# Optimization experiments

Measured on AMD Instinct MI355X. Metric: run time of the kernel, lower is better.

## Reference

```python
import jax, jax.numpy as jnp
import numpy as np

DIM = 128
HEADS = 8
HEAD_DIM = DIM // HEADS
K = 5          # kernel_size per spatial axis
DIL = 1        # dilation
EPS = 1e-5


def setup_inputs() -> dict:
    key = jax.random.key(0)
    ks = jax.random.split(key, 12)
    s = 0.02
    inp = {
        "x": jax.random.normal(ks[0], (1, DIM, 16, 16, 4), jnp.float32),
        "skip": jax.random.normal(ks[1], (1, DIM, 32, 32, 8), jnp.float32),
        "Wq": jax.random.normal(ks[2], (DIM, DIM), jnp.float32) * s,
        "bq": jnp.zeros((DIM,), jnp.float32),
        "Wk": jax.random.normal(ks[3], (DIM, DIM), jnp.float32) * s,
        "bk": jnp.zeros((DIM,), jnp.float32),
        "Wv": jax.random.normal(ks[4], (DIM, DIM), jnp.float32) * s,
        "bv": jnp.zeros((DIM,), jnp.float32),
        "rpb": jax.random.normal(ks[5], (HEADS, 2 * K - 1, 2 * K - 1, 2 * K - 1), jnp.float32) * s,
        "Wo": jax.random.normal(ks[6], (DIM, DIM), jnp.float32) * s,
        "bo": jnp.zeros((DIM,), jnp.float32),
    }
    return inp


def _instance_norm(t):
    # InstanceNorm3d, affine=False: normalize over spatial dims per (B, C)
    mu = jnp.mean(t, axis=(2, 3, 4), keepdims=True)
    var = jnp.var(t, axis=(2, 3, 4), keepdims=True)
    return (t - mu) * jax.lax.rsqrt(var + EPS)


def _nbr_idx(L):
    # NATTEN-style clamped window: start shifted to stay in bounds
    i = np.arange(L)
    start = np.clip(i - (K // 2) * DIL, 0, L - 1 - (K - 1) * DIL)
    idx = start[:, None] + np.arange(K)[None, :] * DIL  # (L, K)
    rel = (idx - i[:, None]) // DIL + (K - 1)           # (L, K) in [0, 2K-2]
    return jnp.asarray(idx), jnp.asarray(rel)


def reference(x, skip, Wq, bq, Wk, bk, Wv, bv, rpb, Wo, bo):
    x = _instance_norm(x)
    skip = _instance_norm(skip)

    xu = jnp.repeat(jnp.repeat(jnp.repeat(x, 2, axis=2), 2, axis=3), 2, axis=4)

    B, C, H, W, Z = skip.shape
    N = H * W * Z
    xt = xu.transpose(0, 2, 3, 4, 1).reshape(B, N, C)    # queries from upsampled x
    st = skip.transpose(0, 2, 3, 4, 1).reshape(B, N, C)  # keys/values from skip

    def heads(t):
        return t.reshape(B, N, HEADS, HEAD_DIM).transpose(0, 2, 1, 3)  # (B,h,N,d)

    q = heads(xt @ Wq + bq) * (HEAD_DIM ** -0.5)
    k = heads(st @ Wk + bk)
    v = heads(st @ Wv + bv)

    idxH, relH = _nbr_idx(H)
    idxW, relW = _nbr_idx(W)
    idxZ, relZ = _nbr_idx(Z)

    # flattened neighbor token indices: (N, K^3)
    nbr = (idxH[:, None, None, :, None, None] * (W * Z)
           + idxW[None, :, None, None, :, None] * Z
           + idxZ[None, None, :, None, None, :])
    nbr = jnp.broadcast_to(nbr, (H, W, Z, K, K, K)).reshape(N, K ** 3)

    # relative position bias gather: (heads, N, K^3)
    rH = jnp.broadcast_to(relH[:, None, None, :, None, None], (H, W, Z, K, K, K)).reshape(N, K ** 3)
    rW = jnp.broadcast_to(relW[None, :, None, None, :, None], (H, W, Z, K, K, K)).reshape(N, K ** 3)
    rZ = jnp.broadcast_to(relZ[None, None, :, None, None, :], (H, W, Z, K, K, K)).reshape(N, K ** 3)
    bias = rpb[:, rH, rW, rZ]  # (heads, N, K^3)

    kg = jnp.take(k, nbr, axis=2)  # (B, h, N, K^3, d)
    vg = jnp.take(v, nbr, axis=2)

    logits = jnp.einsum('bhnd,bhnkd->bhnk', q, kg) + bias[None]
    attn = jax.nn.softmax(logits, axis=-1)
    out = jnp.einsum('bhnk,bhnkd->bhnd', attn, vg)

    out = out.transpose(0, 2, 1, 3).reshape(B, N, C) @ Wo + bo
    return out.reshape(B, H, W, Z, C).transpose(0, 4, 1, 2, 3)
```

## Files before the change

### kernel.cpp

```cpp
#include <hip/hip_runtime.h>
#include <math.h>

#define DIM 128
#define HEADS 8
#define HD 16
#define NPOS 8192
#define EPS 1e-5f

typedef _Float16 half2_t __attribute__((ext_vector_type(2)));
typedef _Float16 f16x8  __attribute__((ext_vector_type(8)));
typedef float    f32x4  __attribute__((ext_vector_type(4)));

static __device__ __forceinline__ half2_t u2h(unsigned u) {
    half2_t r; __builtin_memcpy(&r, &u, 4); return r;
}
static __device__ __forceinline__ unsigned pkh(float a, float b) {
    half2_t h; h.x = (_Float16)a; h.y = (_Float16)b;
    unsigned u; __builtin_memcpy(&u, &h, 4); return u;
}
static __device__ __forceinline__ float dot2(unsigned k, unsigned q, float acc) {
#if __has_builtin(__builtin_amdgcn_fdot2)
    return __builtin_amdgcn_fdot2(u2h(k), u2h(q), acc, false);
#else
    half2_t kh = u2h(k), qh = u2h(q);
    acc = fmaf((float)kh.x, (float)qh.x, acc);
    return fmaf((float)kh.y, (float)qh.y, acc);
#endif
}

__global__ __launch_bounds__(256) void stats_kernel(const float* __restrict__ x,
                                                    const float* __restrict__ skip,
                                                    const float* __restrict__ Wq,
                                                    const float* __restrict__ Wk,
                                                    const float* __restrict__ Wv,
                                                    const float* __restrict__ Wo,
                                                    float* __restrict__ ws,
                                                    unsigned short* __restrict__ Wt) {
    int c = blockIdx.x;
    int t = threadIdx.x;
    if (c >= 256) {
        int c2 = c - 256;
        int m = c2 >> 2, chunk = c2 & 3;
        const float* Wsrc = (m == 0) ? Wq : (m == 1) ? Wk : (m == 2) ? Wv : Wo;
        unsigned short* dst = Wt + (size_t)m * 16384;
        int co = t & 127, half = t >> 7;
        int ci0 = chunk * 32 + half * 16;
        unsigned pk8[8];
        #pragma unroll
        for (int j = 0; j < 8; ++j) {
            float a = Wsrc[(ci0 + 2*j    ) * 128 + co];
            float b = Wsrc[(ci0 + 2*j + 1) * 128 + co];
            pk8[j] = pkh(a, b);
        }
        *(uint4*)(dst + (size_t)co * 128 + ci0)     = *(uint4*)&pk8[0];
        *(uint4*)(dst + (size_t)co * 128 + ci0 + 8) = *(uint4*)&pk8[4];
        return;
    }
    const float* src; int n; float* mu_out; float* rs_out; int ci;
    if (c < DIM) { ci = c; src = x + c * 1024; n = 1024; mu_out = ws; rs_out = ws + DIM; }
    else { ci = c - DIM; src = skip + (size_t)ci * NPOS; n = NPOS; mu_out = ws + 2*DIM; rs_out = ws + 3*DIM; }
    const float4* s4 = (const float4*)src;
    int n4 = n >> 2;
    float s = 0.f, s2 = 0.f;
    for (int i = t; i < n4; i += 256) {
        float4 v = s4[i];
        s += (v.x + v.y) + (v.z + v.w);
        s2 = fmaf(v.x, v.x, fmaf(v.y, v.y, fmaf(v.z, v.z, fmaf(v.w, v.w, s2))));
    }
    #pragma unroll
    for (int off = 32; off > 0; off >>= 1) {
        s  += __shfl_down(s,  off, 64);
        s2 += __shfl_down(s2, off, 64);
    }
    __shared__ float ls[4], ls2[4];
    int wv = t >> 6;
    if ((t & 63) == 0) { ls[wv] = s; ls2[wv] = s2; }
    __syncthreads();
    if (t == 0) {
        float S  = ls[0] + ls[1] + ls[2] + ls[3];
        float S2 = ls2[0] + ls2[1] + ls2[2] + ls2[3];
        float inv_n = 1.f / (float)n;
        float mu  = S * inv_n;
        float var = S2 * inv_n - mu * mu;
        mu_out[ci] = mu;
        rs_out[ci] = rsqrtf(var + EPS);
    }
}

__global__ __launch_bounds__(256) void gemm_kernel(int phase,
    const float* __restrict__ x, const float* __restrict__ skip,
    const float* __restrict__ ao_t,
    const unsigned short* __restrict__ Wt_all,
    const float* __restrict__ bq, const float* __restrict__ bk,
    const float* __restrict__ bv, const float* __restrict__ bo,
    const float* __restrict__ ws,
    unsigned* __restrict__ q_out, unsigned* __restrict__ k_out,
    unsigned* __restrict__ v_out, float* __restrict__ out) {
    __shared__ __align__(16) unsigned short A_lds[32 * 128];
    int bx = blockIdx.x;
    const float* A; int lda; const float* mu; const float* rs;
    const unsigned short* Wt; const float* bias; float scale = 1.f;
    unsigned* opk = nullptr; float* of = nullptr; int n0;
    if (phase == 0) {
        if (bx < 256)      { A = skip; lda = NPOS; mu = ws + 256; rs = ws + 384;
                             Wt = Wt_all + 16384;     bias = bk; opk = k_out; n0 = bx * 32; }
        else if (bx < 512) { A = skip; lda = NPOS; mu = ws + 256; rs = ws + 384;
                             Wt = Wt_all + 2 * 16384; bias = bv; opk = v_out; n0 = (bx - 256) * 32; }
        else               { A = x;    lda = 1024; mu = ws;       rs = ws + 128;
                             Wt = Wt_all;             bias = bq; opk = q_out; n0 = (bx - 512) * 32;
                             scale = 0.25f; }
    } else {
        A = ao_t; lda = NPOS; mu = nullptr; rs = nullptr;
        Wt = Wt_all + 3 * 16384; bias = bo; of = out; n0 = bx * 32;
    }
    int t = threadIdx.x;
    int lane = t & 63, w = t >> 6;

    int co_f = w * 32 + (lane & 15);
    int kf   = (lane >> 4) * 8;
    uint4 wf[2][4];
    #pragma unroll
    for (int mt = 0; mt < 2; ++mt)
        #pragma unroll
        for (int k4 = 0; k4 < 4; ++k4)
            wf[mt][k4] = *(const uint4*)(Wt + (size_t)(co_f + mt * 16) * 128 + k4 * 32 + kf);

    {
        int pos = t & 31, g = t >> 5;
        const float* ap = A + n0 + pos;
        float f[16];
        #pragma unroll
        for (int rep = 0; rep < 4; ++rep) {
            int ci0 = g * 4 + rep * 32;
            f[rep*4+0] = ap[(size_t)(ci0    ) * lda];
            f[rep*4+1] = ap[(size_t)(ci0 + 1) * lda];
            f[rep*4+2] = ap[(size_t)(ci0 + 2) * lda];
            f[rep*4+3] = ap[(size_t)(ci0 + 3) * lda];
        }
        #pragma unroll
        for (int rep = 0; rep < 4; ++rep) {
            int ci0 = g * 4 + rep * 32;
            float f0 = f[rep*4+0], f1 = f[rep*4+1], f2 = f[rep*4+2], f3 = f[rep*4+3];
            if (phase == 0) {
                f0 = (f0 - mu[ci0    ]) * rs[ci0    ];
                f1 = (f1 - mu[ci0 + 1]) * rs[ci0 + 1];
                f2 = (f2 - mu[ci0 + 2]) * rs[ci0 + 2];
                f3 = (f3 - mu[ci0 + 3]) * rs[ci0 + 3];
            }
            int byte = (pos * 256 + ci0 * 2) ^ ((pos & 7) << 4);
            *(uint2*)((char*)A_lds + byte) = make_uint2(pkh(f0, f1), pkh(f2, f3));
        }
    }
    __syncthreads();

    f32x4 acc[2][2];
    #pragma unroll
    for (int mt = 0; mt < 2; ++mt)
        #pragma unroll
        for (int nt = 0; nt < 2; ++nt)
            acc[mt][nt] = (f32x4){0.f, 0.f, 0.f, 0.f};
    #pragma unroll
    for (int k4 = 0; k4 < 4; ++k4) {
        f16x8 af[2];
        #pragma unroll
        for (int nt = 0; nt < 2; ++nt) {
            int pos = nt * 16 + (lane & 15);
            int byte = (pos * 256 + (k4 * 32 + kf) * 2) ^ ((pos & 7) << 4);
            uint4 u = *(const uint4*)((const char*)A_lds + byte);
            __builtin_memcpy(&af[nt], &u, 16);
        }
        #pragma unroll
        for (int mt = 0; mt < 2; ++mt) {
            f16x8 wfr; __builtin_memcpy(&wfr, &wf[mt][k4], 16);
            acc[mt][0] = __builtin_amdgcn_mfma_f32_16x16x32_f16(wfr, af[0], acc[mt][0], 0, 0, 0);
            acc[mt][1] = __builtin_amdgcn_mfma_f32_16x16x32_f16(wfr, af[1], acc[mt][1], 0, 0, 0);
        }
    }

    int colp  = lane & 15;
    int rquad = (lane >> 4) * 4;
    #pragma unroll
    for (int mt = 0; mt < 2; ++mt) {
        int co = w * 32 + mt * 16 + rquad;
        float4 bv4 = *(const float4*)(bias + co);
        #pragma unroll
        for (int nt = 0; nt < 2; ++nt) {
            int pos = n0 + nt * 16 + colp;
            float v0 = (acc[mt][nt][0] + bv4.x) * scale;
            float v1 = (acc[mt][nt][1] + bv4.y) * scale;
            float v2 = (acc[mt][nt][2] + bv4.z) * scale;
            float v3 = (acc[mt][nt][3] + bv4.w) * scale;
            if (phase == 0) {
                *(uint2*)(opk + (size_t)pos * 64 + (co >> 1)) = make_uint2(pkh(v0, v1), pkh(v2, v3));
            } else {
                of[(size_t)(co    ) * NPOS + pos] = v0;
                of[(size_t)(co + 1) * NPOS + pos] = v1;
                of[(size_t)(co + 2) * NPOS + pos] = v2;
                of[(size_t)(co + 3) * NPOS + pos] = v3;
            }
        }
    }
}

__global__ __launch_bounds__(512, 4) void attn_kernel(const unsigned* __restrict__ qb,
                                                      const unsigned* __restrict__ kb,
                                                      const unsigned* __restrict__ vb,
                                                      const float* __restrict__ rpb,
                                                      float* __restrict__ ao_t) {
    __shared__ uint4 kbf[2 * 544];
    __shared__ uint4 vbf[2 * 544];
    __shared__ float bias_l[744];

    int blk = blockIdx.x;
    int h    = blk & 7;
    int tile = blk >> 3;
    int h0 = (tile >> 3) * 4;
    int w0 = (tile & 7) * 4;
    int bh0 = min(max(h0 - 2, 0), 24);
    int bw0 = min(max(w0 - 2, 0), 24);
    int t = threadIdx.x;

    for (int idx = t; idx < 1024; idx += 512) {
        int c2 = idx & 1;
        int r  = idx >> 1;
        int gz = r & 7;
        int q2 = r >> 3;
        int gh = q2 >> 3, gw = q2 & 7;
        int n = (bh0 + gh) * 256 + (bw0 + gw) * 8 + gz;
        int base = gh * 68 + gw * 8 + ((gz + gw) & 7);
        kbf[c2 * 544 + base] = *(const uint4*)(kb + (size_t)n * 64 + h * 8 + c2 * 4);
        vbf[c2 * 544 + base] = *(const uint4*)(vb + (size_t)n * 64 + h * 8 + c2 * 4);
    }
    for (int idx = t; idx < 744; idx += 512) bias_l[idx] = (idx < 729) ? rpb[h * 729 + idx] : 0.f;
    __syncthreads();

    int s = t & 7, p = t >> 3;
    int ph = p >> 4, pw = (p >> 2) & 3, pzp = p & 3;
    int hc = h0 + ph, wc = w0 + pw, zc0 = pzp * 2;
    int sh = min(max(hc - 2, 0), 27);
    int sw = min(max(wc - 2, 0), 27);
    int sz0 = min(max(zc0 - 2, 0), 3);
    int sz1 = min(max(zc0 - 1, 0), 3);
    int dlt = sz1 - sz0;
    int hb = sh - bh0, wb = sw - bw0;
    int b0 = (sh - hc + 4) * 81 + (sw - wc + 4) * 9 + (sz0 - zc0 + 4);
    int n0pos = hc * 256 + wc * 8 + zc0;

    int qrow = (hc >> 1) * 64 + (wc >> 1) * 4 + pzp;
    uint4 qa = *(const uint4*)(qb + (size_t)qrow * 64 + h * 8);
    uint4 qc = *(const uint4*)(qb + (size_t)qrow * 64 + h * 8 + 4);

    float o0[16], o1[16];
    #pragma unroll
    for (int d = 0; d < 16; ++d) { o0[d] = 0.f; o1[d] = 0.f; }
    float l0 = 0.f, l1 = 0.f;

    int cnt   = 18 + (s < 6);
    int start = s * 18 + min(s, 6);
    int i0 = p & 15;

    for (int it = 0; it < cnt; ++it) {
        int ii = i0 + it; if (ii >= cnt) ii -= cnt;
        int j = start + ii;
        int jh = (j * 2185) >> 16;
        int jr = j - jh * 30;
        int jw = (jr * 43) >> 8;
        int jz = jr - jw * 6;
        int gw = wb + jw;
        int gz = sz0 + jz;
        int base = (hb + jh) * 68 + gw * 8 + ((gz + gw) & 7);
        int joff = jh * 81 + jw * 9 + jz;
        float bias1 = bias_l[b0 + joff - 1];
        float bias0 = bias_l[b0 + joff];

        uint4 ka = kbf[base];
        uint4 k2 = kbf[544 + base];
        float d0 = dot2(ka.x, qa.x, 0.f);
        float d1 = dot2(ka.y, qa.y, 0.f);
        d0 = dot2(ka.z, qa.z, d0);
        d1 = dot2(ka.w, qa.w, d1);
        d0 = dot2(k2.x, qc.x, d0);
        d1 = dot2(k2.y, qc.y, d1);
        d0 = dot2(k2.z, qc.z, d0);
        d1 = dot2(k2.w, qc.w, d1);
        float d = d0 + d1;

        bool v0ok = (jz < 5);
        bool v1ok = ((unsigned)(jz - dlt) < 5u);
        float e0 = __expf(d + bias0);
        float e1 = __expf(d + bias1);
        float pp0 = v0ok ? e0 : 0.f;
        float pp1 = v1ok ? e1 : 0.f;
        l0 += pp0; l1 += pp1;

        uint4 va = vbf[base];
        uint4 v2 = vbf[544 + base];
        #define PV(u, dd) { half2_t vh = u2h(u); float f0 = (float)vh.x, f1 = (float)vh.y; \
            o0[dd]   = fmaf(pp0, f0, o0[dd]);   o1[dd]   = fmaf(pp1, f0, o1[dd]); \
            o0[dd+1] = fmaf(pp0, f1, o0[dd+1]); o1[dd+1] = fmaf(pp1, f1, o1[dd+1]); }
        PV(va.x, 0)  PV(va.y, 2)  PV(va.z, 4)  PV(va.w, 6)
        PV(v2.x, 8)  PV(v2.y, 10) PV(v2.z, 12) PV(v2.w, 14)
        #undef PV
    }

    #pragma unroll
    for (int step = 1; step <= 4; step <<= 1) {
        l0 += __shfl_xor(l0, step, 64);
        l1 += __shfl_xor(l1, step, 64);
        #pragma unroll
        for (int d = 0; d < 16; ++d) {
            o0[d] += __shfl_xor(o0[d], step, 64);
            o1[d] += __shfl_xor(o1[d], step, 64);
        }
    }
    float inv0 = 1.f / l0, inv1 = 1.f / l1;
    int row = h * 16 + 2 * s;
    float2 r0 = make_float2(o0[2*s]     * inv0, o1[2*s]     * inv1);
    float2 r1 = make_float2(o0[2*s + 1] * inv0, o1[2*s + 1] * inv1);
    *(float2*)(ao_t + (size_t)row       * NPOS + n0pos) = r0;
    *(float2*)(ao_t + (size_t)(row + 1) * NPOS + n0pos) = r1;
}

extern "C" void kernel_launch(void* const* d_in, const int* in_sizes, int n_in,
                              void* d_out, int out_size, void* d_ws, size_t ws_size,
                              hipStream_t stream) {
    const float* x    = (const float*)d_in[0];
    const float* skip = (const float*)d_in[1];
    const float* Wq   = (const float*)d_in[2];
    const float* bq   = (const float*)d_in[3];
    const float* Wk   = (const float*)d_in[4];
    const float* bk   = (const float*)d_in[5];
    const float* Wv   = (const float*)d_in[6];
    const float* bv   = (const float*)d_in[7];
    const float* rpb  = (const float*)d_in[8];
    const float* Wo   = (const float*)d_in[9];
    const float* bo   = (const float*)d_in[10];
    float* out = (float*)d_out;

    float*          ws  = (float*)d_ws;
    unsigned short* Wt  = (unsigned short*)(ws + 512);
    unsigned* q   = (unsigned*)(Wt + 4 * 16384);
    unsigned* kbp = q + 1024 * 64;
    unsigned* vbp = kbp + (size_t)NPOS * 64;
    float*    ao_t = (float*)(vbp + (size_t)NPOS * 64);

    stats_kernel<<<272, 256, 0, stream>>>(x, skip, Wq, Wk, Wv, Wo, ws, Wt);
    gemm_kernel<<<544, 256, 0, stream>>>(0, x, skip, ao_t, Wt, bq, bk, bv, bo, ws,
                                         q, kbp, vbp, out);
    attn_kernel<<<512, 512, 0, stream>>>(q, kbp, vbp, rpb, ao_t);
    gemm_kernel<<<256, 256, 0, stream>>>(1, x, skip, ao_t, Wt, bq, bk, bv, bo, ws,
                                         q, kbp, vbp, out);
}
```

Measured before the change: 115.7 us.

## Share each query across 2x2 output positions and store attention output as fp16

Each attention thread now serves four output positions (a 2x2 block in w and z) that share one upsampled query, with a 6x6x6 union window. Every key/value load and dot product is therefore reused across four outputs, and the block size drops to 256 threads. The exponent uses exp2 with log2(e) folded into the query scale and the bias. The attention output is written as packed fp16 in token-major layout, so the output GEMM loads it directly with vector loads, cutting traffic. The cost is higher register pressure from 64 accumulators per thread and some masked wasted exponentials.

New measurement: 118.1 us. 2.0% more time.

```diff
diff --git a/kernel.cpp b/kernel.cpp
--- a/kernel.cpp
+++ b/kernel.cpp
@@ -6,6 +6,7 @@
 #define HD 16
 #define NPOS 8192
 #define EPS 1e-5f
+#define RLN2 1.44269504088896f
 
 typedef _Float16 half2_t __attribute__((ext_vector_type(2)));
 typedef _Float16 f16x8  __attribute__((ext_vector_type(8)));
@@ -25,6 +26,13 @@
     half2_t kh = u2h(k), qh = u2h(q);
     acc = fmaf((float)kh.x, (float)qh.x, acc);
     return fmaf((float)kh.y, (float)qh.y, acc);
+#endif
+}
+static __device__ __forceinline__ float ex2(float x) {
+#if __has_builtin(__builtin_amdgcn_exp2f)
+    return __builtin_amdgcn_exp2f(x);
+#else
+    return exp2f(x);
 #endif
 }
 
@@ -89,7 +97,7 @@
 
 __global__ __launch_bounds__(256) void gemm_kernel(int phase,
     const float* __restrict__ x, const float* __restrict__ skip,
-    const float* __restrict__ ao_t,
+    const unsigned* __restrict__ ao_h,
     const unsigned short* __restrict__ Wt_all,
     const float* __restrict__ bq, const float* __restrict__ bk,
     const float* __restrict__ bv, const float* __restrict__ bo,
@@ -98,7 +106,7 @@
     unsigned* __restrict__ v_out, float* __restrict__ out) {
     __shared__ __align__(16) unsigned short A_lds[32 * 128];
     int bx = blockIdx.x;
-    const float* A; int lda; const float* mu; const float* rs;
+    const float* A = nullptr; int lda = 0; const float* mu = nullptr; const float* rs = nullptr;
     const unsigned short* Wt; const float* bias; float scale = 1.f;
     unsigned* opk = nullptr; float* of = nullptr; int n0;
     if (phase == 0) {
@@ -108,9 +116,8 @@
                              Wt = Wt_all + 2 * 16384; bias = bv; opk = v_out; n0 = (bx - 256) * 32; }
         else               { A = x;    lda = 1024; mu = ws;       rs = ws + 128;
                              Wt = Wt_all;             bias = bq; opk = q_out; n0 = (bx - 512) * 32;
-                             scale = 0.25f; }
+                             scale = 0.25f * RLN2; }
     } else {
-        A = ao_t; lda = NPOS; mu = nullptr; rs = nullptr;
         Wt = Wt_all + 3 * 16384; bias = bo; of = out; n0 = bx * 32;
     }
     int t = threadIdx.x;
@@ -125,7 +132,7 @@
         for (int k4 = 0; k4 < 4; ++k4)
             wf[mt][k4] = *(const uint4*)(Wt + (size_t)(co_f + mt * 16) * 128 + k4 * 32 + kf);
 
-    {
+    if (phase == 0) {
         int pos = t & 31, g = t >> 5;
         const float* ap = A + n0 + pos;
         float f[16];
@@ -140,15 +147,19 @@
         #pragma unroll
         for (int rep = 0; rep < 4; ++rep) {
             int ci0 = g * 4 + rep * 32;
-            float f0 = f[rep*4+0], f1 = f[rep*4+1], f2 = f[rep*4+2], f3 = f[rep*4+3];
-            if (phase == 0) {
-                f0 = (f0 - mu[ci0    ]) * rs[ci0    ];
-                f1 = (f1 - mu[ci0 + 1]) * rs[ci0 + 1];
-                f2 = (f2 - mu[ci0 + 2]) * rs[ci0 + 2];
-                f3 = (f3 - mu[ci0 + 3]) * rs[ci0 + 3];
-            }
+            float f0 = (f[rep*4+0] - mu[ci0    ]) * rs[ci0    ];
+            float f1 = (f[rep*4+1] - mu[ci0 + 1]) * rs[ci0 + 1];
+            float f2 = (f[rep*4+2] - mu[ci0 + 2]) * rs[ci0 + 2];
+            float f3 = (f[rep*4+3] - mu[ci0 + 3]) * rs[ci0 + 3];
             int byte = (pos * 256 + ci0 * 2) ^ ((pos & 7) << 4);
             *(uint2*)((char*)A_lds + byte) = make_uint2(pkh(f0, f1), pkh(f2, f3));
+        }
+    } else {
+        for (int i = t; i < 512; i += 256) {
+            int pos = i >> 4, j = i & 15;
+            uint4 u = *(const uint4*)(ao_h + (size_t)(n0 + pos) * 64 + j * 4);
+            int byte = (pos * 256 + j * 16) ^ ((pos & 7) << 4);
+            *(uint4*)((char*)A_lds + byte) = u;
         }
     }
     __syncthreads();
@@ -202,11 +213,11 @@
     }
 }
 
-__global__ __launch_bounds__(512, 4) void attn_kernel(const unsigned* __restrict__ qb,
+__global__ __launch_bounds__(256, 2) void attn_kernel(const unsigned* __restrict__ qb,
                                                       const unsigned* __restrict__ kb,
                                                       const unsigned* __restrict__ vb,
                                                       const float* __restrict__ rpb,
-                                                      float* __restrict__ ao_t) {
+                                                      unsigned* __restrict__ ao_h) {
     __shared__ uint4 kbf[2 * 544];
     __shared__ uint4 vbf[2 * 544];
     __shared__ float bias_l[744];
@@ -220,7 +231,15 @@
     int bw0 = min(max(w0 - 2, 0), 24);
     int t = threadIdx.x;
 
-    for (int idx = t; idx < 1024; idx += 512) {
+    for (int idx = t; idx < 64; idx += 256) {
+        int half = idx & 1;
+        int r = idx >> 1;
+        int row = r >> 2, cpad = r & 3;
+        int off = half * 544 + row * 68 + 64 + cpad;
+        kbf[off] = make_uint4(0u, 0u, 0u, 0u);
+        vbf[off] = make_uint4(0u, 0u, 0u, 0u);
+    }
+    for (int idx = t; idx < 1024; idx += 256) {
         int c2 = idx & 1;
         int r  = idx >> 1;
         int gz = r & 7;
@@ -231,47 +250,60 @@
         kbf[c2 * 544 + base] = *(const uint4*)(kb + (size_t)n * 64 + h * 8 + c2 * 4);
         vbf[c2 * 544 + base] = *(const uint4*)(vb + (size_t)n * 64 + h * 8 + c2 * 4);
     }
-    for (int idx = t; idx < 744; idx += 512) bias_l[idx] = (idx < 729) ? rpb[h * 729 + idx] : 0.f;
+    for (int idx = t; idx < 744; idx += 256)
+        bias_l[idx] = (idx < 729) ? rpb[h * 729 + idx] * RLN2 : 0.f;
     __syncthreads();
 
     int s = t & 7, p = t >> 3;
-    int ph = p >> 4, pw = (p >> 2) & 3, pzp = p & 3;
-    int hc = h0 + ph, wc = w0 + pw, zc0 = pzp * 2;
-    int sh = min(max(hc - 2, 0), 27);
-    int sw = min(max(wc - 2, 0), 27);
+    int ph = p >> 3, pw2 = (p >> 2) & 1, pz2 = p & 3;
+    int hc  = h0 + ph;
+    int wc0 = w0 + pw2 * 2;
+    int zc0 = pz2 * 2;
+    int sh  = min(max(hc - 2, 0), 27);
+    int sw0 = min(max(wc0 - 2, 0), 27);
+    int sw1 = min(max(wc0 - 1, 0), 27);
+    int dw  = sw1 - sw0;
     int sz0 = min(max(zc0 - 2, 0), 3);
     int sz1 = min(max(zc0 - 1, 0), 3);
-    int dlt = sz1 - sz0;
-    int hb = sh - bh0, wb = sw - bw0;
-    int b0 = (sh - hc + 4) * 81 + (sw - wc + 4) * 9 + (sz0 - zc0 + 4);
-    int n0pos = hc * 256 + wc * 8 + zc0;
-
-    int qrow = (hc >> 1) * 64 + (wc >> 1) * 4 + pzp;
+    int dz  = sz1 - sz0;
+    int hb = sh - bh0, wb = sw0 - bw0;
+    int b0 = (sh - hc + 4) * 81 + (sw0 - wc0 + 4) * 9 + (sz0 - zc0 + 4);
+    int n00 = hc * 256 + wc0 * 8 + zc0;
+
+    int qrow = (hc >> 1) * 64 + (wc0 >> 1) * 4 + pz2;
     uint4 qa = *(const uint4*)(qb + (size_t)qrow * 64 + h * 8);
     uint4 qc = *(const uint4*)(qb + (size_t)qrow * 64 + h * 8 + 4);
 
-    float o0[16], o1[16];
-    #pragma unroll
-    for (int d = 0; d < 16; ++d) { o0[d] = 0.f; o1[d] = 0.f; }
-    float l0 = 0.f, l1 = 0.f;
-
-    int cnt   = 18 + (s < 6);
-    int start = s * 18 + min(s, 6);
+    float o[4][16];
+    float l[4];
+    #pragma unroll
+    for (int qq = 0; qq < 4; ++qq) {
+        l[qq] = 0.f;
+        #pragma unroll
+        for (int d = 0; d < 16; ++d) o[qq][d] = 0.f;
+    }
+
+    int cnt   = 22 + (s < 4);
+    int start = s * 22 + min(s, 4);
     int i0 = p & 15;
 
     for (int it = 0; it < cnt; ++it) {
         int ii = i0 + it; if (ii >= cnt) ii -= cnt;
         int j = start + ii;
-        int jh = (j * 2185) >> 16;
-        int jr = j - jh * 30;
+        int jh = (j * 1821) >> 16;
+        int jr = j - jh * 36;
         int jw = (jr * 43) >> 8;
         int jz = jr - jw * 6;
-        int gw = wb + jw;
-        int gz = sz0 + jz;
-        int base = (hb + jh) * 68 + gw * 8 + ((gz + gw) & 7);
-        int joff = jh * 81 + jw * 9 + jz;
-        float bias1 = bias_l[b0 + joff - 1];
-        float bias0 = bias_l[b0 + joff];
+        int gww = wb + jw;
+        int gz  = sz0 + jz;
+        int gwc = min(gww, 7);
+        int gzc = min(gz, 7);
+        int base = (hb + jh) * 68 + gwc * 8 + ((gzc + gwc) & 7);
+        int bidx = b0 + jh * 81 + jw * 9 + jz;
+        float b11 = bias_l[bidx - 10];
+        float b10 = bias_l[bidx - 9];
+        float b01 = bias_l[bidx - 1];
+        float b00 = bias_l[bidx];
 
         uint4 ka = kbf[base];
         uint4 k2 = kbf[544 + base];
@@ -285,19 +317,23 @@
         d1 = dot2(k2.w, qc.w, d1);
         float d = d0 + d1;
 
-        bool v0ok = (jz < 5);
-        bool v1ok = ((unsigned)(jz - dlt) < 5u);
-        float e0 = __expf(d + bias0);
-        float e1 = __expf(d + bias1);
-        float pp0 = v0ok ? e0 : 0.f;
-        float pp1 = v1ok ? e1 : 0.f;
-        l0 += pp0; l1 += pp1;
+        bool vw0 = (jw < 5);
+        bool vw1 = ((unsigned)(jw - dw) < 5u);
+        bool vz0 = (jz < 5);
+        bool vz1 = ((unsigned)(jz - dz) < 5u);
+        float p00 = (vw0 && vz0) ? ex2(d + b00) : 0.f;
+        float p01 = (vw0 && vz1) ? ex2(d + b01) : 0.f;
+        float p10 = (vw1 && vz0) ? ex2(d + b10) : 0.f;
+        float p11 = (vw1 && vz1) ? ex2(d + b11) : 0.f;
+        l[0] += p00; l[1] += p01; l[2] += p10; l[3] += p11;
 
         uint4 va = vbf[base];
         uint4 v2 = vbf[544 + base];
         #define PV(u, dd) { half2_t vh = u2h(u); float f0 = (float)vh.x, f1 = (float)vh.y; \
-            o0[dd]   = fmaf(pp0, f0, o0[dd]);   o1[dd]   = fmaf(pp1, f0, o1[dd]); \
-            o0[dd+1] = fmaf(pp0, f1, o0[dd+1]); o1[dd+1] = fmaf(pp1, f1, o1[dd+1]); }
+            o[0][dd] = fmaf(p00, f0, o[0][dd]); o[0][dd+1] = fmaf(p00, f1, o[0][dd+1]); \
+            o[1][dd] = fmaf(p01, f0, o[1][dd]); o[1][dd+1] = fmaf(p01, f1, o[1][dd+1]); \
+            o[2][dd] = fmaf(p10, f0, o[2][dd]); o[2][dd+1] = fmaf(p10, f1, o[2][dd+1]); \
+            o[3][dd] = fmaf(p11, f0, o[3][dd]); o[3][dd+1] = fmaf(p11, f1, o[3][dd+1]); }
         PV(va.x, 0)  PV(va.y, 2)  PV(va.z, 4)  PV(va.w, 6)
         PV(v2.x, 8)  PV(v2.y, 10) PV(v2.z, 12) PV(v2.w, 14)
         #undef PV
@@ -305,20 +341,20 @@
 
     #pragma unroll
     for (int step = 1; step <= 4; step <<= 1) {
-        l0 += __shfl_xor(l0, step, 64);
-        l1 += __shfl_xor(l1, step, 64);
-        #pragma unroll
-        for (int d = 0; d < 16; ++d) {
-            o0[d] += __shfl_xor(o0[d], step, 64);
-            o1[d] += __shfl_xor(o1[d], step, 64);
-        }
-    }
-    float inv0 = 1.f / l0, inv1 = 1.f / l1;
-    int row = h * 16 + 2 * s;
-    float2 r0 = make_float2(o0[2*s]     * inv0, o1[2*s]     * inv1);
-    float2 r1 = make_float2(o0[2*s + 1] * inv0, o1[2*s + 1] * inv1);
-    *(float2*)(ao_t + (size_t)row       * NPOS + n0pos) = r0;
-    *(float2*)(ao_t + (size_t)(row + 1) * NPOS + n0pos) = r1;
+        #pragma unroll
+        for (int qq = 0; qq < 4; ++qq) {
+            l[qq] += __shfl_xor(l[qq], step, 64);
+            #pragma unroll
+            for (int d = 0; d < 16; ++d) o[qq][d] += __shfl_xor(o[qq][d], step, 64);
+        }
+    }
+    int ci = h * 8 + s;
+    #pragma unroll
+    for (int qq = 0; qq < 4; ++qq) {
+        float inv = 1.f / l[qq];
+        int pos = n00 + (qq >> 1) * 8 + (qq & 1);
+        ao_h[(size_t)pos * 64 + ci] = pkh(o[qq][2*s] * inv, o[qq][2*s+1] * inv);
+    }
 }
 
 extern "C" void kernel_launch(void* const* d_in, const int* in_sizes, int n_in,
@@ -339,15 +375,15 @@
 
     float*          ws  = (float*)d_ws;
     unsigned short* Wt  = (unsigned short*)(ws + 512);
-    unsigned* q   = (unsigned*)(Wt + 4 * 16384);
-    unsigned* kbp = q + 1024 * 64;
-    unsigned* vbp = kbp + (size_t)NPOS * 64;
-    float*    ao_t = (float*)(vbp + (size_t)NPOS * 64);
+    unsigned* q    = (unsigned*)(Wt + 4 * 16384);
+    unsigned* kbp  = q + 1024 * 64;
+    unsigned* vbp  = kbp + (size_t)NPOS * 64;
+    unsigned* ao_h = vbp + (size_t)NPOS * 64;
 
     stats_kernel<<<272, 256, 0, stream>>>(x, skip, Wq, Wk, Wv, Wo, ws, Wt);
-    gemm_kernel<<<544, 256, 0, stream>>>(0, x, skip, ao_t, Wt, bq, bk, bv, bo, ws,
+    gemm_kernel<<<544, 256, 0, stream>>>(0, x, skip, ao_h, Wt, bq, bk, bv, bo, ws,
                                          q, kbp, vbp, out);
-    attn_kernel<<<512, 512, 0, stream>>>(q, kbp, vbp, rpb, ao_t);
-    gemm_kernel<<<256, 256, 0, stream>>>(1, x, skip, ao_t, Wt, bq, bk, bv, bo, ws,
+    attn_kernel<<<512, 256, 0, stream>>>(q, kbp, vbp, rpb, ao_h);
+    gemm_kernel<<<256, 256, 0, stream>>>(1, x, skip, ao_h, Wt, bq, bk, bv, bo, ws,
                                          q, kbp, vbp, out);
 }
```
